# Optimization experiments

Measured on AMD Instinct MI355X. Metric: run time of the kernel, lower is better.

## Reference

```python
import jax, jax.numpy as jnp
import numpy as np

RADIUS = 1.3
COARSE = 64
FINE = 2
N_ATOMS = 64
SH_DIM = 9
DATA_DIM = SH_DIM * 3 + 1  # 28
N_INTRS = COARSE * 3 * 2 * FINE  # 768
STEP = (RADIUS * 2.0 / COARSE / FINE) / 2.0
BATCH = 1024


def sh_basis(d):
    # real spherical harmonics basis, degree 2 (9 coeffs), on normalized dirs
    d = d / jnp.linalg.norm(d, axis=-1, keepdims=True)
    x, y, z = d[..., 0], d[..., 1], d[..., 2]
    C0 = 0.28209479177387814
    C1 = 0.4886025119029199
    C20, C21, C22, C23, C24 = (1.0925484305920792, -1.0925484305920792,
                               0.31539156525252005, -1.0925484305920792,
                               0.5462742152960396)
    return jnp.stack([
        C0 * jnp.ones_like(x), -C1 * y, C1 * z, -C1 * x,
        C20 * x * y, C21 * y * z, C22 * (2.0 * z * z - x * x - y * y),
        C23 * x * z, C24 * (x * x - y * y)
    ], axis=-1)


def dict_interp(grid, atoms, pts):
    # l2_interp_v2: coarse-voxel dictionary coeffs x trilinear fine-atom interp
    # pts: [P,3] in [0,1)
    P = pts.shape[0]
    pc = pts * COARSE
    c = jnp.clip(jnp.floor(pc), 0, COARSE - 1).astype(jnp.int32)
    local = pc - c.astype(pts.dtype)  # position inside coarse voxel, [0,1)
    clin = (c[:, 0] * COARSE + c[:, 1]) * COARSE + c[:, 2]
    coeff = grid[clin]                              # [P, A]
    # project dictionary coeffs through atoms for every fine cell: [P, FINE^3, D]
    proj = jnp.einsum('pa,fad->pfd', coeff, atoms)
    u = local * FINE - 0.5
    f = jnp.floor(u)
    t = u - f
    i0 = jnp.clip(f, 0, FINE - 1).astype(jnp.int32)
    i1 = jnp.clip(f + 1.0, 0, FINE - 1).astype(jnp.int32)
    idx = jnp.stack([i0, i1], axis=-1)              # [P,3,2]
    w = jnp.stack([1.0 - t, t], axis=-1)            # [P,3,2]
    rows = jnp.arange(P)
    out = jnp.zeros((P, DATA_DIM), dtype=pts.dtype)
    for kx in (0, 1):
        for ky in (0, 1):
            for kz in (0, 1):
                lin = (idx[:, 0, kx] * FINE + idx[:, 1, ky]) * FINE + idx[:, 2, kz]
                wgt = w[:, 0, kx] * w[:, 1, ky] * w[:, 2, kz]
                out = out + wgt[:, None] * proj[rows, lin]
    return out


def _forward(rays_o, rays_d, grid, atoms):
    dt = rays_o.dtype
    # ---- sample_proposal (no grad) ----
    off_pos = (RADIUS - rays_o) / rays_d
    off_neg = (-RADIUS - rays_o) / rays_d
    start = jnp.max(jnp.minimum(off_pos, off_neg), axis=-1, keepdims=True)
    intersections = jax.lax.stop_gradient(
        start + jnp.arange(N_INTRS, dtype=dt)[None, :] * STEP)  # [B, 768]
    tr = intersections[:, :-1]  # [B, 767]
    pts = rays_o[:, None, :] + tr[..., None] * rays_d[:, None, :]  # [B,n,3]
    mask = jnp.all((pts > -RADIUS) & (pts < RADIUS), axis=-1)      # [B,n]
    pts = jax.lax.stop_gradient(pts)
    B, n = tr.shape
    # normalized coords in [0,1); masked-out points are clipped then zeroed later
    p = jnp.clip((pts + RADIUS) / (2.0 * RADIUS), 0.0, 1.0 - 1e-6).reshape(-1, 3)
    data = dict_interp(grid, atoms, p).reshape(B, n, DATA_DIM)
    # masked_scatter of sigma <=> dense compute + where(mask, ., 0)
    sigma = jnp.where(mask, jax.nn.relu(data[..., -1]), 0.0)
    dists = (intersections[:, 1:] - intersections[:, :-1]) * \
        jnp.linalg.norm(rays_d, axis=-1, keepdims=True)
    alpha = 1.0 - jnp.exp(-sigma * dists)
    trans = jnp.cumprod(1.0 - alpha + 1e-10, axis=-1)
    trans = jnp.concatenate([jnp.ones_like(trans[:, :1]), trans[:, :-1]], axis=-1)
    abs_light = alpha * trans  # per-sample weights
    sh_mult = sh_basis(rays_d)                      # [B, 9]
    sh = data[..., :-1].reshape(B, n, 3, SH_DIM)
    rgb_samp = jnp.einsum('bnck,bk->bnc', sh, sh_mult)
    rgb_samp = jax.nn.sigmoid(jnp.where(mask[..., None], rgb_samp, 0.0))
    comp = jnp.sum(abs_light[..., None] * rgb_samp, axis=1)  # [B,3]
    acc = jnp.sum(abs_light, axis=1)
    rgb = comp + (1.0 - acc)[:, None]  # white background
    depth = jnp.sum(abs_light * tr, axis=1)
    return rgb, alpha, depth


def setup_inputs():
    key = jax.random.key(0)
    k0, k1, k2, k3 = jax.random.split(key, 4)
    o = jax.random.normal(k0, (BATCH, 3), dtype=jnp.float32)
    o = o / jnp.linalg.norm(o, axis=-1, keepdims=True) * 2.5
    d = -o + 0.3 * jax.random.normal(k1, (BATCH, 3), dtype=jnp.float32)
    d = d / jnp.linalg.norm(d, axis=-1, keepdims=True)
    grid = 0.01 * jax.random.normal(k2, (COARSE ** 3, N_ATOMS), dtype=jnp.float32)
    atoms_sh = jax.random.uniform(k3, (FINE ** 3, N_ATOMS, DATA_DIM - 1), dtype=jnp.float32)
    atoms = jnp.concatenate(
        [atoms_sh, jnp.full((FINE ** 3, N_ATOMS, 1), 0.01, dtype=jnp.float32)], axis=-1)
    return {"rays_o": o, "rays_d": d, "grid": grid, "atoms": atoms, "grid_id": 0}


def reference(rays_o, rays_d, grid, atoms, grid_id):
    # grid_id selects among num_scenes grids; num_scenes=1 so grid is pre-selected
    return _forward(rays_o, rays_d, grid, atoms)
```

## Files before the change

kernel.cpp:

```cpp
#include <hip/hip_runtime.h>
#include <hip/hip_bf16.h>

#define RADIUS_F 1.3f
#define NSAMP 767
#define STEPF 0.01015625f
#define BATCH 1024

typedef __attribute__((ext_vector_type(8))) short short8;
typedef __attribute__((ext_vector_type(4))) float floatx4;
typedef __attribute__((ext_vector_type(4))) unsigned uintx4;
typedef __fp16 fp16x2 __attribute__((ext_vector_type(2)));

static __device__ __forceinline__ unsigned pkbf(float a, float b) {
    union { __hip_bfloat162 h; unsigned u; } cvt;
    cvt.h = __float22bfloat162_rn(make_float2(a, b));
    return cvt.u;
}
static __device__ __forceinline__ unsigned pkh(float a, float b) {
    union { fp16x2 h; unsigned u; } c;
    c.h = __builtin_amdgcn_cvt_pkrtz(a, b);
    return c.u;
}
static __device__ __forceinline__ float2 uph(unsigned u) {
    union { unsigned u; fp16x2 h; } c; c.u = u;
    return make_float2((float)c.h.x, (float)c.h.y);
}

static __device__ __forceinline__ float coset4_sum(float p) {
    int q4 = __builtin_amdgcn_update_dpp(0, __float_as_int(p), 0x124, 0xf, 0xf, true);
    p = p + __int_as_float(q4);
    int q8 = __builtin_amdgcn_update_dpp(0, __float_as_int(p), 0x128, 0xf, 0xf, true);
    return p + __int_as_float(q8);
}

__launch_bounds__(512, 6)
__global__ void plenoxels_fwd(const float* __restrict__ rays_o,
                              const float* __restrict__ rays_d,
                              const float* __restrict__ grid,
                              const float* __restrict__ atoms,
                              float* __restrict__ out)
{
    __shared__ __align__(16) __hip_bfloat16 BpL[32 * 72];
    __shared__ __align__(16) unsigned WtU[4 * 776];
    __shared__ __align__(16) float pAct[768 * 4];
    __shared__ int clinL[768];
    __shared__ float wprodL[8];
    __shared__ float partL[8][5];

    const int tid  = threadIdx.x;
    const int ray  = blockIdx.x;
    const int lane = tid & 63;
    const int w    = tid >> 6;
    const int m    = lane & 15;
    const int quad = lane >> 4;

    const float ox = rays_o[ray * 3 + 0], oy = rays_o[ray * 3 + 1], oz = rays_o[ray * 3 + 2];
    const float dx = rays_d[ray * 3 + 0], dy = rays_d[ray * 3 + 1], dz = rays_d[ray * 3 + 2];

    float start, exitT;
    {
        float a0 = (RADIUS_F - ox) / dx, b0 = (-RADIUS_F - ox) / dx;
        float a1 = (RADIUS_F - oy) / dy, b1 = (-RADIUS_F - oy) / dy;
        float a2 = (RADIUS_F - oz) / dz, b2 = (-RADIUS_F - oz) / dz;
        start = fmaxf(fminf(a0, b0), fmaxf(fminf(a1, b1), fminf(a2, b2)));
        exitT = fminf(fmaxf(a0, b0), fminf(fmaxf(a1, b1), fmaxf(a2, b2)));
    }
    const float dnorm = sqrtf(dx * dx + dy * dy + dz * dz);
    const float dist = STEPF * dnorm;

    int nAct;
    {
        float span = (exitT - start) / STEPF;
        if (span >= 0.f) nAct = (span < 765.f) ? ((int)span + 2) : NSAMP;
        else             nAct = (span < 0.f) ? 0 : NSAMP;
    }
    const int seg = ((nAct + 127) >> 7) << 4;
    const int nT  = seg >> 4;

    auto geom = [&](int s) {
        float tr = start + (float)s * STEPF;
        float px = ox + tr * dx, py = oy + tr * dy, pz = oz + tr * dz;
        int mask = (px > -RADIUS_F) & (px < RADIUS_F) &
                   (py > -RADIUS_F) & (py < RADIUS_F) &
                   (pz > -RADIUS_F) & (pz < RADIUS_F) & (s < NSAMP);
        float maskf = mask ? 1.f : 0.f;
        const float sc = 1.0f / (2.0f * RADIUS_F);
        float qx = fminf(fmaxf((px + RADIUS_F) * sc, 0.f), 1.0f - 1e-6f);
        float qy = fminf(fmaxf((py + RADIUS_F) * sc, 0.f), 1.0f - 1e-6f);
        float qz = fminf(fmaxf((pz + RADIUS_F) * sc, 0.f), 1.0f - 1e-6f);
        float pcx = qx * 64.f, pcy = qy * 64.f, pcz = qz * 64.f;
        float cx = fminf(floorf(pcx), 63.f);
        float cy = fminf(floorf(pcy), 63.f);
        float cz = fminf(floorf(pcz), 63.f);
        float lx = pcx - cx, ly = pcy - cy, lz = pcz - cz;
        int clin = (((int)cx * 64) + (int)cy) * 64 + (int)cz;
        float xw0, xw1, yw0, yw1, zw0, zw1;
        {
            float u = lx * 2.f - 0.5f, fF = floorf(u), t = u - fF;
            xw0 = (fF < 0.f) ? 1.f : ((fF > 0.f) ? 0.f : 1.f - t);
            xw1 = (fF < 0.f) ? 0.f : ((fF > 0.f) ? 1.f : t);
        }
        {
            float u = ly * 2.f - 0.5f, fF = floorf(u), t = u - fF;
            yw0 = (fF < 0.f) ? 1.f : ((fF > 0.f) ? 0.f : 1.f - t);
            yw1 = (fF < 0.f) ? 0.f : ((fF > 0.f) ? 1.f : t);
        }
        {
            float u = lz * 2.f - 0.5f, fF = floorf(u), t = u - fF;
            zw0 = (fF < 0.f) ? 1.f : ((fF > 0.f) ? 0.f : 1.f - t);
            zw1 = (fF < 0.f) ? 0.f : ((fF > 0.f) ? 1.f : t);
        }
        xw0 *= maskf; xw1 *= maskf;
        float g0 = yw0 * zw0, g1 = yw0 * zw1, g2 = yw1 * zw0, g3 = yw1 * zw1;
        WtU[       s] = pkh(xw0 * g0, xw1 * g0);
        WtU[ 776 + s] = pkh(xw0 * g1, xw1 * g1);
        WtU[1552 + s] = pkh(xw0 * g2, xw1 * g2);
        WtU[2328 + s] = pkh(xw0 * g3, xw1 * g3);
        clinL[s] = clin;
    };

    if (lane < seg)      geom(w * seg + lane);
    if (lane + 64 < seg) geom(w * seg + 64 + lane);

    const float4* g4 = (const float4*)grid;
    float4 cv0 = {0,0,0,0}, cv1 = {0,0,0,0}, cv2 = {0,0,0,0}, cv3 = {0,0,0,0};
    if (nT > 0) {
        int clinC = clinL[w * seg + m];
        const float4* gp = g4 + (clinC << 4) + (quad << 2);
        cv0 = gp[0]; cv1 = gp[1]; cv2 = gp[2]; cv3 = gp[3];
    }

    {
        float shm[9];
        float inv = 1.0f / dnorm;
        float nx = dx * inv, ny = dy * inv, nz = dz * inv;
        shm[0] = 0.28209479177387814f;
        shm[1] = -0.4886025119029199f * ny;
        shm[2] = 0.4886025119029199f * nz;
        shm[3] = -0.4886025119029199f * nx;
        shm[4] = 1.0925484305920792f * nx * ny;
        shm[5] = -1.0925484305920792f * ny * nz;
        shm[6] = 0.31539156525252005f * (2.f * nz * nz - nx * nx - ny * ny);
        shm[7] = -1.0925484305920792f * nx * nz;
        shm[8] = 0.5462742152960396f * (nx * nx - ny * ny);

        const float* base = atoms + tid * 28;
        float4 v0 = *(const float4*)(base);
        float4 v1 = *(const float4*)(base + 4);
        float4 v2 = *(const float4*)(base + 8);
        float4 v3 = *(const float4*)(base + 12);
        float4 v4 = *(const float4*)(base + 16);
        float4 v5 = *(const float4*)(base + 20);
        float4 v6 = *(const float4*)(base + 24);

        float s0 = v0.x*shm[0] + v0.y*shm[1] + v0.z*shm[2] + v0.w*shm[3]
                 + v1.x*shm[4] + v1.y*shm[5] + v1.z*shm[6] + v1.w*shm[7] + v2.x*shm[8];
        float s1 = v2.y*shm[0] + v2.z*shm[1] + v2.w*shm[2] + v3.x*shm[3]
                 + v3.y*shm[4] + v3.z*shm[5] + v3.w*shm[6] + v4.x*shm[7] + v4.y*shm[8];
        float s2 = v4.z*shm[0] + v4.w*shm[1] + v5.x*shm[2] + v5.y*shm[3]
                 + v5.z*shm[4] + v5.w*shm[5] + v6.x*shm[6] + v6.y*shm[7] + v6.z*shm[8];

        int f = tid >> 6, a = tid & 63;
        int cb = (f << 2) * 72 + a;
        BpL[cb]        = __float2bfloat16(s0);
        BpL[cb + 72]   = __float2bfloat16(s1);
        BpL[cb + 144]  = __float2bfloat16(s2);
        BpL[cb + 216]  = __float2bfloat16(v6.w);
    }
    __syncthreads();

    short8 bq00, bq01, bq10, bq11;
    {
        const short* bs = (const short*)BpL;
        const short* p0 = bs + m * 72 + (quad << 4);
        bq00 = *(const short8*)(p0);
        bq01 = *(const short8*)(p0 + 8);
        const short* p1 = bs + (16 + m) * 72 + (quad << 4);
        bq10 = *(const short8*)(p1);
        bq11 = *(const short8*)(p1 + 8);
    }

    float* out_rgb   = out;
    float* out_alpha = out + BATCH * 3;
    float* out_depth = out + BATCH * 3 + BATCH * NSAMP;
    const int f0 = m >> 2;

    #pragma unroll
    for (int t = 0; t < 6; ++t) {
        if (t >= nT) break;

        union { unsigned u[4]; short8 s; } a0p, a1p;
        a0p.u[0] = pkbf(cv0.x, cv0.y); a0p.u[1] = pkbf(cv0.z, cv0.w);
        a0p.u[2] = pkbf(cv1.x, cv1.y); a0p.u[3] = pkbf(cv1.z, cv1.w);
        a1p.u[0] = pkbf(cv2.x, cv2.y); a1p.u[1] = pkbf(cv2.z, cv2.w);
        a1p.u[2] = pkbf(cv3.x, cv3.y); a1p.u[3] = pkbf(cv3.z, cv3.w);

        if (t + 1 < nT) {
            int clinC = clinL[w * seg + ((t + 1) << 4) + m];
            const float4* gp = g4 + (clinC << 4) + (quad << 2);
            cv0 = gp[0]; cv1 = gp[1]; cv2 = gp[2]; cv3 = gp[3];
        }

        floatx4 acc0 = {0.f, 0.f, 0.f, 0.f};
        floatx4 acc1 = {0.f, 0.f, 0.f, 0.f};
        acc0 = __builtin_amdgcn_mfma_f32_16x16x32_bf16(a0p.s, bq00, acc0, 0, 0, 0);
        acc0 = __builtin_amdgcn_mfma_f32_16x16x32_bf16(a1p.s, bq01, acc0, 0, 0, 0);
        acc1 = __builtin_amdgcn_mfma_f32_16x16x32_bf16(a0p.s, bq10, acc1, 0, 0, 0);
        acc1 = __builtin_amdgcn_mfma_f32_16x16x32_bf16(a1p.s, bq11, acc1, 0, 0, 0);

        int sb = w * seg + (t << 4) + (quad << 2);
        union { uintx4 v; unsigned u[4]; } wt;
        wt.v = *(const uintx4*)&WtU[f0 * 776 + sb];
        #pragma unroll
        for (int r = 0; r < 4; ++r) {
            float2 wab = uph(wt.u[r]);
            float p = wab.x * acc0[r] + wab.y * acc1[r];
            p = coset4_sum(p);
            if (m < 4) {
                float e = __expf((m == 3) ? (-fmaxf(p, 0.f) * dist) : -p);
                float v = (m == 3) ? (1.f - e) : (1.f / (1.f + e));
                pAct[((sb + r) << 2) + m] = v;
            }
        }
    }

    __syncthreads();

    {
        const int sLim = seg << 3;
        const bool act = (tid < 384);
        const int s0 = tid * 2;
        float a0 = 0.f, a1 = 0.f;
        float r0 = 0.f, g0c = 0.f, b0c = 0.f, r1 = 0.f, g1c = 0.f, b1c = 0.f;
        if (act) {
            if (s0 < sLim) {
                float4 q = *(const float4*)&pAct[s0 << 2];
                r0 = q.x; g0c = q.y; b0c = q.z; a0 = q.w;
            }
            if (s0 + 1 < sLim) {
                float4 q = *(const float4*)&pAct[(s0 + 1) << 2];
                r1 = q.x; g1c = q.y; b1c = q.z; a1 = q.w;
            }
            out_alpha[ray * NSAMP + s0] = a0;
            if (s0 + 1 < NSAMP) out_alpha[ray * NSAMP + s0 + 1] = a1;
        }
        float pr = (1.f - a0 + 1e-10f) * (1.f - a1 + 1e-10f);

        float incl = pr;
        #pragma unroll
        for (int off = 1; off < 64; off <<= 1) {
            float v = __shfl_up(incl, off, 64);
            if (lane >= off) incl *= v;
        }
        if (lane == 63) wprodL[w] = incl;
        __syncthreads();

        float base = 1.f;
        #pragma unroll
        for (int ww = 0; ww < 5; ++ww)
            if (w > ww) base *= wprodL[ww];
        float excl = __shfl_up(incl, 1, 64);
        if (lane == 0) excl = 1.f;
        float trans = base * excl;

        float c0 = 0.f, c1 = 0.f, c2 = 0.f, accw = 0.f, dep = 0.f;
        if (act) {
            float w0 = a0 * trans;
            c0 += w0 * r0; c1 += w0 * g0c; c2 += w0 * b0c;
            accw += w0;
            dep += w0 * (start + (float)s0 * STEPF);
            trans *= (1.f - a0 + 1e-10f);
            float w1 = a1 * trans;
            c0 += w1 * r1; c1 += w1 * g1c; c2 += w1 * b1c;
            accw += w1;
            dep += w1 * (start + (float)(s0 + 1) * STEPF);
        }
        #pragma unroll
        for (int off = 1; off < 64; off <<= 1) {
            c0   += __shfl_xor(c0, off, 64);
            c1   += __shfl_xor(c1, off, 64);
            c2   += __shfl_xor(c2, off, 64);
            accw += __shfl_xor(accw, off, 64);
            dep  += __shfl_xor(dep, off, 64);
        }
        if (lane == 0) {
            partL[w][0] = c0; partL[w][1] = c1; partL[w][2] = c2;
            partL[w][3] = accw; partL[w][4] = dep;
        }
        __syncthreads();
        if (tid == 0) {
            float C0 = 0.f, C1 = 0.f, C2 = 0.f, AC = 0.f, DP = 0.f;
            #pragma unroll
            for (int ww = 0; ww < 6; ++ww) {
                C0 += partL[ww][0]; C1 += partL[ww][1]; C2 += partL[ww][2];
                AC += partL[ww][3]; DP += partL[ww][4];
            }
            float bg = 1.f - AC;
            out_rgb[ray * 3 + 0] = C0 + bg;
            out_rgb[ray * 3 + 1] = C1 + bg;
            out_rgb[ray * 3 + 2] = C2 + bg;
            out_depth[ray] = DP;
        }
    }
}

extern "C" void kernel_launch(void* const* d_in, const int* in_sizes, int n_in,
                              void* d_out, int out_size, void* d_ws, size_t ws_size,
                              hipStream_t stream) {
    const float* rays_o = (const float*)d_in[0];
    const float* rays_d = (const float*)d_in[1];
    const float* grid   = (const float*)d_in[2];
    const float* atoms  = (const float*)d_in[3];
    float* out = (float*)d_out;
    hipLaunchKernelGGL(plenoxels_fwd, dim3(BATCH), dim3(512), 0, stream,
                       rays_o, rays_d, grid, atoms, out);
}
```

Measured before the change: 111.9 us.

## Fuse volume-rendering compositing into MFMA loop, drop shared activation buffer

```diff
diff --git a/kernel.cpp b/kernel.cpp
--- a/kernel.cpp
+++ b/kernel.cpp
@@ -42,7 +42,6 @@
 {
     __shared__ __align__(16) __hip_bfloat16 BpL[32 * 72];
     __shared__ __align__(16) unsigned WtU[4 * 776];
-    __shared__ __align__(16) float pAct[768 * 4];
     __shared__ int clinL[768];
     __shared__ float wprodL[8];
     __shared__ float partL[8][5];
@@ -184,6 +183,11 @@
     float* out_alpha = out + BATCH * 3;
     float* out_depth = out + BATCH * 3 + BATCH * NSAMP;
     const int f0 = m >> 2;
+    const int c3 = ((m & 3) == 3);
+
+    float cacc = 0.f;
+    float accw = 0.f, dep = 0.f;
+    float R = 1.f;
 
     #pragma unroll
     for (int t = 0; t < 6; ++t) {
@@ -211,96 +215,81 @@
         int sb = w * seg + (t << 4) + (quad << 2);
         union { uintx4 v; unsigned u[4]; } wt;
         wt.v = *(const uintx4*)&WtU[f0 * 776 + sb];
+        float va[4];
         #pragma unroll
         for (int r = 0; r < 4; ++r) {
             float2 wab = uph(wt.u[r]);
             float p = wab.x * acc0[r] + wab.y * acc1[r];
             p = coset4_sum(p);
-            if (m < 4) {
-                float e = __expf((m == 3) ? (-fmaxf(p, 0.f) * dist) : -p);
-                float v = (m == 3) ? (1.f - e) : (1.f / (1.f + e));
-                pAct[((sb + r) << 2) + m] = v;
-            }
-        }
-    }
+            float e = __expf(c3 ? (-fmaxf(p, 0.f) * dist) : -p);
+            va[r] = c3 ? (1.f - e) : (1.f / (1.f + e));
+        }
+
+        float q0 = 1.f - va[0] + 1e-10f;
+        float q1 = 1.f - va[1] + 1e-10f;
+        float q2 = 1.f - va[2] + 1e-10f;
+        float q3 = 1.f - va[3] + 1e-10f;
+        float t1 = q0, t2 = q0 * q1, t3 = q0 * q1 * q2;
+        float P  = t3 * q3;
+        float incl = P;
+        float u16 = __shfl_up(incl, 16, 64); if (quad >= 1) incl *= u16;
+        float u32 = __shfl_up(incl, 32, 64); if (quad >= 2) incl *= u32;
+        float Eq  = __shfl_up(incl, 16, 64); if (quad == 0) Eq = 1.f;
+        float tbase = R * Eq;
+        float w0 = va[0] * tbase;
+        float w1 = va[1] * tbase * t1;
+        float w2 = va[2] * tbase * t2;
+        float w3 = va[3] * tbase * t3;
+        R *= __shfl(incl, 63, 64);
+
+        if (m == 3) {
+            float s0f = start + (float)sb * STEPF;
+            accw += w0 + w1 + w2 + w3;
+            dep  += w0 * s0f + w1 * (s0f + STEPF)
+                  + w2 * (s0f + 2.f * STEPF) + w3 * (s0f + 3.f * STEPF);
+            int o = ray * NSAMP + sb;
+            out_alpha[o] = va[0];
+            if (sb + 1 < NSAMP) out_alpha[o + 1] = va[1];
+            if (sb + 2 < NSAMP) out_alpha[o + 2] = va[2];
+            if (sb + 3 < NSAMP) out_alpha[o + 3] = va[3];
+        }
+
+        #pragma unroll
+        for (int r = 0; r < 4; ++r) {
+            float wr = (r == 0) ? w0 : (r == 1) ? w1 : (r == 2) ? w2 : w3;
+            int wb = __builtin_amdgcn_update_dpp(0, __float_as_int(wr), 0xFF, 0xF, 0xF, true);
+            if (m < 3) cacc += __int_as_float(wb) * va[r];
+        }
+    }
+
+    #pragma unroll
+    for (int off = 4; off <= 32; off <<= 1) {
+        cacc += __shfl_xor(cacc, off, 64);
+        accw += __shfl_xor(accw, off, 64);
+        dep  += __shfl_xor(dep,  off, 64);
+    }
+    if (lane < 3)  partL[w][lane] = cacc;
+    if (lane == 3) { partL[w][3] = accw; partL[w][4] = dep; }
+    if (lane == 0) wprodL[w] = R;
+
+    for (int s = (seg << 3) + tid; s < NSAMP; s += 512)
+        out_alpha[ray * NSAMP + s] = 0.f;
 
     __syncthreads();
 
-    {
-        const int sLim = seg << 3;
-        const bool act = (tid < 384);
-        const int s0 = tid * 2;
-        float a0 = 0.f, a1 = 0.f;
-        float r0 = 0.f, g0c = 0.f, b0c = 0.f, r1 = 0.f, g1c = 0.f, b1c = 0.f;
-        if (act) {
-            if (s0 < sLim) {
-                float4 q = *(const float4*)&pAct[s0 << 2];
-                r0 = q.x; g0c = q.y; b0c = q.z; a0 = q.w;
-            }
-            if (s0 + 1 < sLim) {
-                float4 q = *(const float4*)&pAct[(s0 + 1) << 2];
-                r1 = q.x; g1c = q.y; b1c = q.z; a1 = q.w;
-            }
-            out_alpha[ray * NSAMP + s0] = a0;
-            if (s0 + 1 < NSAMP) out_alpha[ray * NSAMP + s0 + 1] = a1;
-        }
-        float pr = (1.f - a0 + 1e-10f) * (1.f - a1 + 1e-10f);
-
-        float incl = pr;
+    if (tid == 0) {
+        float C0 = 0.f, C1 = 0.f, C2 = 0.f, AC = 0.f, DP = 0.f, B = 1.f;
         #pragma unroll
-        for (int off = 1; off < 64; off <<= 1) {
-            float v = __shfl_up(incl, off, 64);
-            if (lane >= off) incl *= v;
-        }
-        if (lane == 63) wprodL[w] = incl;
-        __syncthreads();
-
-        float base = 1.f;
-        #pragma unroll
-        for (int ww = 0; ww < 5; ++ww)
-            if (w > ww) base *= wprodL[ww];
-        float excl = __shfl_up(incl, 1, 64);
-        if (lane == 0) excl = 1.f;
-        float trans = base * excl;
-
-        float c0 = 0.f, c1 = 0.f, c2 = 0.f, accw = 0.f, dep = 0.f;
-        if (act) {
-            float w0 = a0 * trans;
-            c0 += w0 * r0; c1 += w0 * g0c; c2 += w0 * b0c;
-            accw += w0;
-            dep += w0 * (start + (float)s0 * STEPF);
-            trans *= (1.f - a0 + 1e-10f);
-            float w1 = a1 * trans;
-            c0 += w1 * r1; c1 += w1 * g1c; c2 += w1 * b1c;
-            accw += w1;
-            dep += w1 * (start + (float)(s0 + 1) * STEPF);
-        }
-        #pragma unroll
-        for (int off = 1; off < 64; off <<= 1) {
-            c0   += __shfl_xor(c0, off, 64);
-            c1   += __shfl_xor(c1, off, 64);
-            c2   += __shfl_xor(c2, off, 64);
-            accw += __shfl_xor(accw, off, 64);
-            dep  += __shfl_xor(dep, off, 64);
-        }
-        if (lane == 0) {
-            partL[w][0] = c0; partL[w][1] = c1; partL[w][2] = c2;
-            partL[w][3] = accw; partL[w][4] = dep;
-        }
-        __syncthreads();
-        if (tid == 0) {
-            float C0 = 0.f, C1 = 0.f, C2 = 0.f, AC = 0.f, DP = 0.f;
-            #pragma unroll
-            for (int ww = 0; ww < 6; ++ww) {
-                C0 += partL[ww][0]; C1 += partL[ww][1]; C2 += partL[ww][2];
-                AC += partL[ww][3]; DP += partL[ww][4];
-            }
-            float bg = 1.f - AC;
-            out_rgb[ray * 3 + 0] = C0 + bg;
-            out_rgb[ray * 3 + 1] = C1 + bg;
-            out_rgb[ray * 3 + 2] = C2 + bg;
-            out_depth[ray] = DP;
-        }
+        for (int ww = 0; ww < 8; ++ww) {
+            C0 += B * partL[ww][0]; C1 += B * partL[ww][1]; C2 += B * partL[ww][2];
+            AC += B * partL[ww][3]; DP += B * partL[ww][4];
+            B  *= wprodL[ww];
+        }
+        float bg = 1.f - AC;
+        out_rgb[ray * 3 + 0] = C0 + bg;
+        out_rgb[ray * 3 + 1] = C1 + bg;
+        out_rgb[ray * 3 + 2] = C2 + bg;
+        out_depth[ray] = DP;
     }
 }
 
```

Measured after the change: 123.1 us. +10.0%, slower.
